# Kernel tuning notes

Hardware: AMD Instinct MI355X
Metric: run time of the kernel (lower is better)

Reference implementation:

```python
import jax, jax.numpy as jnp
import numpy as np

B, DEC, ENC, HID, UNITS = 4, 256, 1024, 512, 128


def setup_inputs() -> dict:
    key = jax.random.key(0)
    k1, k2, k3, k4, k5, k6 = jax.random.split(key, 6)
    query = jax.random.normal(k1, (B, DEC, HID), dtype=jnp.float32)
    value = jax.random.normal(k2, (B, ENC, HID), dtype=jnp.float32)
    mask = jax.random.bernoulli(k3, 0.9, (B, ENC))  # bool, True = keep
    # Dense(units, use_bias=False) kernels, glorot-ish scaling
    W1 = jax.random.normal(k4, (HID, UNITS), dtype=jnp.float32) * (1.0 / np.sqrt(HID))
    W2 = jax.random.normal(k5, (HID, UNITS), dtype=jnp.float32) * (1.0 / np.sqrt(HID))
    # AdditiveAttention use_scale=True: learned per-unit scale vector
    scale = jax.random.normal(k6, (UNITS,), dtype=jnp.float32) * (1.0 / np.sqrt(UNITS))
    return {"query": query, "value": value, "mask": mask, "W1": W1, "W2": W2, "scale": scale}


def reference(query, value, mask, W1, W2, scale):
    # query: (B, DEC, HID), value: (B, ENC, HID), mask: (B, ENC) bool
    q = jnp.einsum("bqh,hu->bqu", query, W1)   # (B, DEC, U)
    k = jnp.einsum("beh,hu->beu", value, W2)   # (B, ENC, U)
    # Bahdanau additive score: sum_u scale_u * tanh(q + k)  -> (B, DEC, ENC)
    scores = jnp.einsum("bqeu,u->bqe", jnp.tanh(q[:, :, None, :] + k[:, None, :, :]), scale)
    neg = jnp.asarray(-1e9, scores.dtype)
    scores = jnp.where(mask[:, None, :], scores, neg)
    attention_weights = jax.nn.softmax(scores, axis=-1)   # (B, DEC, ENC)
    context_vector = jnp.einsum("bqe,beh->bqh", attention_weights, value)  # (B, DEC, HID)
    # query_mask is all-ones in the original module -> no-op on output
    return (context_vector, attention_weights)
```

## Files before the change

### kernel.cpp

```cpp
#include <hip/hip_runtime.h>
#include <cstddef>

#define B     4
#define DEC   256
#define ENC   1024
#define HID   512
#define UNITS 128

#define PROJ_SCALE 2.8853900817779268f

__global__ __launch_bounds__(256) void proj_kernel(
    const float* __restrict__ query, const float* __restrict__ value,
    const float* __restrict__ W1,    const float* __restrict__ W2,
    float* __restrict__ qbuf,        float* __restrict__ kbufT)
{
    __shared__ float part[4][8][UNITS];

    const int tid  = threadIdx.x;
    const int lane = tid & 63;
    const int wv   = __builtin_amdgcn_readfirstlane(tid >> 6);
    const int row0g = blockIdx.x * 8;
    const bool isQ = row0g < B * DEC;
    const float* X = isQ ? query : value;
    const float* W = isQ ? W1 : W2;
    const int row0 = isQ ? row0g : row0g - B * DEC;
    const int h0   = wv * 128;

    float acc0[8], acc1[8];
    #pragma unroll
    for (int r = 0; r < 8; ++r) { acc0[r] = 0.f; acc1[r] = 0.f; }

    const float* Xb = X + (size_t)row0 * HID + h0;
    const float* Wb = W + (size_t)h0 * UNITS;

    float2 wv2[4];
    #pragma unroll
    for (int j = 0; j < 4; ++j)
        wv2[j] = *(const float2*)(Wb + j * UNITS + 2 * lane);

    for (int h = 0; h < 128; h += 4) {
        const int hp = (h + 4 < 128) ? h + 4 : h;
        float2 nv[4];
        #pragma unroll
        for (int j = 0; j < 4; ++j)
            nv[j] = *(const float2*)(Wb + (hp + j) * UNITS + 2 * lane);

        #pragma unroll
        for (int r = 0; r < 8; ++r) {
            const float4 xv = *(const float4*)(Xb + r * HID + h);
            acc0[r] += xv.x*wv2[0].x + xv.y*wv2[1].x + xv.z*wv2[2].x + xv.w*wv2[3].x;
            acc1[r] += xv.x*wv2[0].y + xv.y*wv2[1].y + xv.z*wv2[2].y + xv.w*wv2[3].y;
        }
        #pragma unroll
        for (int j = 0; j < 4; ++j) wv2[j] = nv[j];
    }

    #pragma unroll
    for (int r = 0; r < 8; ++r)
        *(float2*)&part[wv][r][2 * lane] = make_float2(acc0[r], acc1[r]);
    __syncthreads();

    #pragma unroll
    for (int k = 0; k < 4; ++k) {
        const int idx = tid + k * 256;
        const int r = idx >> 7, u = idx & (UNITS - 1);
        const float s = PROJ_SCALE *
            ((part[0][r][u] + part[1][r][u]) + (part[2][r][u] + part[3][r][u]));
        const float z = __builtin_amdgcn_exp2f(s);
        const int row = row0 + r;
        if (isQ) {
            qbuf[(size_t)row * UNITS + u] = z;
        } else {
            const int bb = row >> 10, e = row & (ENC - 1);
            const int c = u >> 2, j = u & 3;
            kbufT[((size_t)bb * 32 * ENC + (size_t)c * ENC + e) * 4 + j] = z;
        }
    }
}

__device__ __forceinline__ float quad_term(const float4 q, const float4 k,
                                           const float4 s) {
    const float A  = fmaf(q.x, k.x, 1.f);
    const float B_ = fmaf(q.y, k.y, 1.f);
    const float C  = fmaf(q.z, k.z, 1.f);
    const float D  = fmaf(q.w, k.w, 1.f);
    const float AB = A * B_, CD = C * D;
    const float n1 = fmaf(s.x, B_, s.y * A);
    const float n2 = fmaf(s.z, D,  s.w * C);
    const float num = fmaf(n1, CD, n2 * AB);
    return num * __builtin_amdgcn_rcpf(AB * CD);
}

__global__ __launch_bounds__(1024) void score_kernel(
    const float* __restrict__ qbuf, const float* __restrict__ kbufT,
    const int* __restrict__ mask,   const float* __restrict__ scale,
    float* __restrict__ attn_out)
{
    const int bi  = blockIdx.x;
    const int b   = (bi >> 1) & 3;
    const int dq0 = (((bi >> 3) << 1) | (bi & 1)) * 4;
    const int tid = threadIdx.x;

    const int m = mask[b * ENC + tid];

    float S0 = 0.f;
    for (int j = 0; j < UNITS; j += 4) {
        const float4 sv = *(const float4*)(scale + j);
        S0 += (sv.x + sv.y) + (sv.z + sv.w);
    }

    const float* q0 = qbuf + (size_t)(b * DEC + dq0) * UNITS;
    const float* kc = kbufT + (size_t)b * 32 * ENC * 4 + (size_t)tid * 4;

    float t0 = 0.f, t1 = 0.f, t2 = 0.f, t3 = 0.f;

    float4 kv = *(const float4*)kc;
    for (int i = 0; i < 32; ++i) {
        float4 nkv;
        if (i + 1 < 32) nkv = *(const float4*)(kc + (size_t)(i + 1) * ENC * 4);
        const float4 sv = *(const float4*)(scale + i * 4);
        const float4 qa = *(const float4*)(q0 + 0 * UNITS + i * 4);
        const float4 qb = *(const float4*)(q0 + 1 * UNITS + i * 4);
        const float4 qc = *(const float4*)(q0 + 2 * UNITS + i * 4);
        const float4 qd = *(const float4*)(q0 + 3 * UNITS + i * 4);

        t0 += quad_term(qa, kv, sv);
        t1 += quad_term(qb, kv, sv);
        t2 += quad_term(qc, kv, sv);
        t3 += quad_term(qd, kv, sv);

        if (i + 1 < 32) kv = nkv;
    }

    float wgt[4];
    wgt[0] = m ? __expf(S0 - 2.f * t0) : 0.f;
    wgt[1] = m ? __expf(S0 - 2.f * t1) : 0.f;
    wgt[2] = m ? __expf(S0 - 2.f * t2) : 0.f;
    wgt[3] = m ? __expf(S0 - 2.f * t3) : 0.f;

    __shared__ float reds[4][16];
    const int lane = tid & 63, wv = tid >> 6;

    float ls[4] = {wgt[0], wgt[1], wgt[2], wgt[3]};
    #pragma unroll
    for (int off = 32; off > 0; off >>= 1) {
        #pragma unroll
        for (int r = 0; r < 4; ++r)
            ls[r] += __shfl_down(ls[r], off, 64);
    }
    if (lane == 0) {
        #pragma unroll
        for (int r = 0; r < 4; ++r) reds[r][wv] = ls[r];
    }
    __syncthreads();
    #pragma unroll
    for (int r = 0; r < 4; ++r) {
        float g = 0.f;
        #pragma unroll
        for (int w = 0; w < 16; ++w) g += reds[r][w];
        attn_out[(size_t)(b * DEC + dq0 + r) * ENC + tid] =
            wgt[r] * __builtin_amdgcn_rcpf(g);
    }
}

__global__ __launch_bounds__(512) void ctx_kernel(
    const float* __restrict__ attn, const float* __restrict__ value,
    float* __restrict__ ctx)
{
    __shared__ float attnS[8][ENC];
    __shared__ float part[8][8][128];

    const int bi   = blockIdx.x;
    const int b    = (bi >> 1) & 3;
    const int idx  = ((bi >> 3) << 1) | (bi & 1);
    const int row0 = (idx >> 2) * 8;
    const int h0   = (idx & 3) * 128;
    const int tid  = threadIdx.x;
    const int lane = tid & 63;
    const int wv   = __builtin_amdgcn_readfirstlane(tid >> 6);

    const float* ab = attn + (size_t)(b * DEC + row0) * ENC;
    #pragma unroll
    for (int k = 0; k < 4; ++k) {
        const float4 v = *(const float4*)(ab + (size_t)k * 2048 + tid * 4);
        *(float4*)&attnS[0][k * 2048 + tid * 4] = v;
    }
    __syncthreads();

    float acc[8][2];
    #pragma unroll
    for (int r = 0; r < 8; ++r) { acc[r][0] = 0.f; acc[r][1] = 0.f; }

    const float* vb = value + (size_t)b * ENC * HID + h0 + lane * 2;
    const int e0 = wv * 128;

    float2 va[4];
    #pragma unroll
    for (int j = 0; j < 4; ++j)
        va[j] = *(const float2*)(vb + (size_t)(e0 + j) * HID);

    for (int g = 0; g < 32; ++g) {
        const int gp = (g + 1 < 32) ? g + 1 : g;
        float2 vn[4];
        #pragma unroll
        for (int j = 0; j < 4; ++j)
            vn[j] = *(const float2*)(vb + (size_t)(e0 + gp * 4 + j) * HID);

        const int eg = e0 + g * 4;
        float4 w4[8];
        #pragma unroll
        for (int r = 0; r < 8; ++r)
            w4[r] = *(const float4*)&attnS[r][eg];

        #pragma unroll
        for (int j = 0; j < 4; ++j) {
            const float2 v2 = va[j];
            #pragma unroll
            for (int r = 0; r < 8; ++r) {
                const float w = ((const float*)&w4[r])[j];
                acc[r][0] += w * v2.x;
                acc[r][1] += w * v2.y;
            }
        }
        #pragma unroll
        for (int j = 0; j < 4; ++j) va[j] = vn[j];
    }

    #pragma unroll
    for (int r = 0; r < 8; ++r)
        *(float2*)&part[wv][r][lane * 2] = make_float2(acc[r][0], acc[r][1]);
    __syncthreads();

    #pragma unroll
    for (int k = 0; k < 2; ++k) {
        const int idx2 = tid + k * 512;
        const int r = idx2 >> 7, hh = idx2 & 127;
        float s = 0.f;
        #pragma unroll
        for (int w = 0; w < 8; ++w) s += part[w][r][hh];
        ctx[(size_t)(b * DEC + row0 + r) * HID + h0 + hh] = s;
    }
}

extern "C" void kernel_launch(void* const* d_in, const int* in_sizes, int n_in,
                              void* d_out, int out_size, void* d_ws, size_t ws_size,
                              hipStream_t stream) {
    const float* query = (const float*)d_in[0];
    const float* value = (const float*)d_in[1];
    const int*   mask  = (const int*)  d_in[2];
    const float* W1    = (const float*)d_in[3];
    const float* W2    = (const float*)d_in[4];
    const float* scale = (const float*)d_in[5];

    float* qbuf  = (float*)d_ws;
    float* kbufT = qbuf + (size_t)B * DEC * UNITS;

    float* ctx_out  = (float*)d_out;
    float* attn_out = ctx_out + (size_t)B * DEC * HID;

    proj_kernel <<<640,  256, 0, stream>>>(query, value, W1, W2, qbuf, kbufT);
    score_kernel<<<256, 1024, 0, stream>>>(qbuf, kbufT, mask, scale, attn_out);
    ctx_kernel  <<<512,  512, 0, stream>>>(attn_out, value, ctx_out);
}
```

Baseline: 129.1 us.

## Stage projection input rows in LDS, deepen weight prefetch, drop softmax constant

The projection kernel now loads its 8 input rows into shared memory once with coalesced float4 loads, then reads them from LDS instead of issuing strided global loads per wave. The weight prefetch is deepened to two steps ahead, and the accumulation is written as explicit fmaf chains. The score kernel no longer computes the sum of the scale vector, because that constant offset cancels in the softmax normalisation. The costs are extra LDS use, a block barrier and a few more registers; the constant removal also raises the risk of exp overflow if scores are large.

```diff
diff --git a/kernel.cpp b/kernel.cpp
--- a/kernel.cpp
+++ b/kernel.cpp
@@ -14,6 +14,7 @@
     const float* __restrict__ W1,    const float* __restrict__ W2,
     float* __restrict__ qbuf,        float* __restrict__ kbufT)
 {
+    __shared__ float xs[8][HID];
     __shared__ float part[4][8][UNITS];
 
     const int tid  = threadIdx.x;
@@ -26,33 +27,49 @@
     const int row0 = isQ ? row0g : row0g - B * DEC;
     const int h0   = wv * 128;
 
+    {
+        const float* xb = X + (size_t)row0 * HID;
+        #pragma unroll
+        for (int k = 0; k < 4; ++k) {
+            const float4 v = *(const float4*)(xb + (size_t)k * 1024 + tid * 4);
+            *(float4*)&xs[0][k * 1024 + tid * 4] = v;
+        }
+    }
+    __syncthreads();
+
     float acc0[8], acc1[8];
     #pragma unroll
     for (int r = 0; r < 8; ++r) { acc0[r] = 0.f; acc1[r] = 0.f; }
 
-    const float* Xb = X + (size_t)row0 * HID + h0;
-    const float* Wb = W + (size_t)h0 * UNITS;
-
-    float2 wv2[4];
-    #pragma unroll
-    for (int j = 0; j < 4; ++j)
-        wv2[j] = *(const float2*)(Wb + j * UNITS + 2 * lane);
+    const float* Wb = W + (size_t)h0 * UNITS + 2 * lane;
+
+    float2 wcur[4], wnxt[4];
+    #pragma unroll
+    for (int j = 0; j < 4; ++j) wcur[j] = *(const float2*)(Wb + j * UNITS);
+    #pragma unroll
+    for (int j = 0; j < 4; ++j) wnxt[j] = *(const float2*)(Wb + (4 + j) * UNITS);
 
     for (int h = 0; h < 128; h += 4) {
-        const int hp = (h + 4 < 128) ? h + 4 : h;
-        float2 nv[4];
+        const int hp = (h + 8 < 128) ? h + 8 : h;
+        float2 np[4];
         #pragma unroll
         for (int j = 0; j < 4; ++j)
-            nv[j] = *(const float2*)(Wb + (hp + j) * UNITS + 2 * lane);
+            np[j] = *(const float2*)(Wb + (hp + j) * UNITS);
 
         #pragma unroll
         for (int r = 0; r < 8; ++r) {
-            const float4 xv = *(const float4*)(Xb + r * HID + h);
-            acc0[r] += xv.x*wv2[0].x + xv.y*wv2[1].x + xv.z*wv2[2].x + xv.w*wv2[3].x;
-            acc1[r] += xv.x*wv2[0].y + xv.y*wv2[1].y + xv.z*wv2[2].y + xv.w*wv2[3].y;
-        }
-        #pragma unroll
-        for (int j = 0; j < 4; ++j) wv2[j] = nv[j];
+            const float4 xv = *(const float4*)&xs[r][h0 + h];
+            acc0[r] = fmaf(xv.x, wcur[0].x, acc0[r]);
+            acc1[r] = fmaf(xv.x, wcur[0].y, acc1[r]);
+            acc0[r] = fmaf(xv.y, wcur[1].x, acc0[r]);
+            acc1[r] = fmaf(xv.y, wcur[1].y, acc1[r]);
+            acc0[r] = fmaf(xv.z, wcur[2].x, acc0[r]);
+            acc1[r] = fmaf(xv.z, wcur[2].y, acc1[r]);
+            acc0[r] = fmaf(xv.w, wcur[3].x, acc0[r]);
+            acc1[r] = fmaf(xv.w, wcur[3].y, acc1[r]);
+        }
+        #pragma unroll
+        for (int j = 0; j < 4; ++j) { wcur[j] = wnxt[j]; wnxt[j] = np[j]; }
     }
 
     #pragma unroll
@@ -103,12 +120,6 @@
 
     const int m = mask[b * ENC + tid];
 
-    float S0 = 0.f;
-    for (int j = 0; j < UNITS; j += 4) {
-        const float4 sv = *(const float4*)(scale + j);
-        S0 += (sv.x + sv.y) + (sv.z + sv.w);
-    }
-
     const float* q0 = qbuf + (size_t)(b * DEC + dq0) * UNITS;
     const float* kc = kbufT + (size_t)b * 32 * ENC * 4 + (size_t)tid * 4;
 
@@ -133,10 +144,10 @@
     }
 
     float wgt[4];
-    wgt[0] = m ? __expf(S0 - 2.f * t0) : 0.f;
-    wgt[1] = m ? __expf(S0 - 2.f * t1) : 0.f;
-    wgt[2] = m ? __expf(S0 - 2.f * t2) : 0.f;
-    wgt[3] = m ? __expf(S0 - 2.f * t3) : 0.f;
+    wgt[0] = m ? __expf(-2.f * t0) : 0.f;
+    wgt[1] = m ? __expf(-2.f * t1) : 0.f;
+    wgt[2] = m ? __expf(-2.f * t2) : 0.f;
+    wgt[3] = m ? __expf(-2.f * t3) : 0.f;
 
     __shared__ float reds[4][16];
     const int lane = tid & 63, wv = tid >> 6;
```

Measured after the change: 123.3 us, median of 2. -4.5%, faster.
